# Performance work log

Measured on AMD Instinct MI355X. Metric: run time of the kernel, lower is better.

## Reference

```python
import jax, jax.numpy as jnp
import numpy as np

N, C, H, W = 2, 128, 64, 64
N_HEAD = 4
GROUPS = 16
EPS = 1e-5


def group_norm(x, scale, offset):
    # haiku GroupNorm, channels_first: normalize over (channels-in-group, h, w)
    n, c, h, w = x.shape
    xg = x.reshape(n, GROUPS, c // GROUPS, h, w)
    mu = xg.mean(axis=(2, 3, 4), keepdims=True)
    var = xg.var(axis=(2, 3, 4), keepdims=True)
    xg = (xg - mu) * jax.lax.rsqrt(var + EPS)
    return xg.reshape(n, c, h, w) * scale[None, :, None, None] + offset[None, :, None, None]


def setup_inputs() -> dict:
    key = jax.random.key(0)
    ks = jax.random.split(key, 4)
    inv_sqrt_c = 1.0 / np.sqrt(C).astype(np.float32)
    return {
        "x": jax.random.normal(ks[0], (N, C, H, W), dtype=jnp.float32),
        "w_qkv": jax.random.normal(ks[1], (C, 3 * C), dtype=jnp.float32) * inv_sqrt_c,
        "b_qkv": jnp.zeros((3 * C,), dtype=jnp.float32),
        "w_out": jax.random.normal(ks[2], (C, C), dtype=jnp.float32) * inv_sqrt_c,
        "b_out": jnp.zeros((C,), dtype=jnp.float32),
        "gn1_scale": jnp.ones((C,), dtype=jnp.float32),
        "gn1_offset": jnp.zeros((C,), dtype=jnp.float32),
        "gn2_scale": jnp.ones((C,), dtype=jnp.float32),
        "gn2_offset": jnp.zeros((C,), dtype=jnp.float32),
    }


def reference(x, w_qkv, b_qkv, w_out, b_out, gn1_scale, gn1_offset, gn2_scale, gn2_offset):
    n, c, h, w = x.shape
    dh = c // N_HEAD
    # GroupNorm (x is reassigned, so the residual uses the normalized x)
    xn = group_norm(x, gn1_scale, gn1_offset)
    # 1x1 conv qkv projection: [n, 3c, h, w]
    qkv = jnp.einsum('nchw,cd->ndhw', xn, w_qkv) + b_qkv[None, :, None, None]
    # [n, 3H, dh, hw] -> [n, 3H, hw, dh]
    qkv = jnp.swapaxes(qkv.reshape(n, N_HEAD * 3, dh, h * w), 2, 3)
    q, k, v = jnp.split(qkv, 3, axis=1)  # each [n, H, hw, dh]
    scale = dh ** (-0.25)
    # [n, H, hw, hw] attention matrix (the memory-bound core)
    att = jax.nn.softmax((q * scale) @ (jnp.swapaxes(k, 2, 3) * scale), axis=3)
    y = jnp.swapaxes(att @ v, 2, 3).reshape(n, c, h, w)
    # 1x1 conv out projection + GroupNorm + residual
    out = jnp.einsum('nchw,cd->ndhw', y, w_out) + b_out[None, :, None, None]
    return xn + group_norm(out, gn2_scale, gn2_offset)
```

## Files before the change

### kernel.cpp

```cpp
#include <hip/hip_runtime.h>
#include <hip/hip_bf16.h>
#include <math.h>

constexpr int cHW   = 4096;
constexpr int cC    = 128;
constexpr int cNH   = 4;
constexpr int cDH   = 32;
constexpr float cEPS = 1e-5f;
constexpr float cQS = 0.2550347805f;
constexpr int SPLIT = 8;

typedef short bh8 __attribute__((ext_vector_type(8)));
typedef float f4  __attribute__((ext_vector_type(4)));

static __device__ __forceinline__ unsigned short f2bf(float f) {
  union { __hip_bfloat16 h; unsigned short u; } cv;
  cv.h = __float2bfloat16(f);
  return cv.u;
}
static __device__ __forceinline__ unsigned pack2bf(float a, float b) {
  return (unsigned)f2bf(a) | ((unsigned)f2bf(b) << 16);
}
static __device__ __forceinline__ unsigned pack_trunc(float a, float b) {
  unsigned ua = __builtin_bit_cast(unsigned, a);
  unsigned ub = __builtin_bit_cast(unsigned, b);
  return (ua >> 16) | (ub & 0xffff0000u);
}
static __device__ __forceinline__ float bflo(unsigned pk) {
  return __builtin_bit_cast(float, pk << 16);
}
static __device__ __forceinline__ float bfhi(unsigned pk) {
  return __builtin_bit_cast(float, pk & 0xffff0000u);
}

__device__ __forceinline__ void block_reduce2(float& a, float& b, float* sbuf) {
  #pragma unroll
  for (int off = 32; off > 0; off >>= 1) {
    a += __shfl_down(a, off, 64);
    b += __shfl_down(b, off, 64);
  }
  int wave = threadIdx.x >> 6;
  int lane = threadIdx.x & 63;
  if (lane == 0) { sbuf[wave] = a; sbuf[4 + wave] = b; }
  __syncthreads();
  if (threadIdx.x == 0) {
    sbuf[8] = sbuf[0] + sbuf[1] + sbuf[2] + sbuf[3];
    sbuf[9] = sbuf[4] + sbuf[5] + sbuf[6] + sbuf[7];
  }
  __syncthreads();
  a = sbuf[8];
  b = sbuf[9];
}

__global__ __launch_bounds__(256)
void prep(const float* __restrict__ x, float* __restrict__ part,
          const float* __restrict__ wq, const float* __restrict__ wo,
          unsigned short* __restrict__ wqT, unsigned short* __restrict__ woT) {
  __shared__ float lds[32 * 133];
  int L = threadIdx.x;
  if (blockIdx.x < 256) {
    int ng = blockIdx.x >> 3, sl = blockIdx.x & 7;
    const float4* s4 = (const float4*)x;
    float s = 0.f, s2 = 0.f;
    #pragma unroll
    for (int i = 0; i < 4; i++) {
      int idx = i * 256 + L;
      int c = idx >> 7, tt = idx & 127;
      float4 v = s4[(size_t)(ng * 8 + c) * 1024 + sl * 128 + tt];
      s  += v.x + v.y + v.z + v.w;
      s2 += v.x*v.x + v.y*v.y + v.z*v.z + v.w*v.w;
    }
    block_reduce2(s, s2, lds);
    if (L == 0) { part[blockIdx.x * 2] = s; part[blockIdx.x * 2 + 1] = s2; }
  } else {
    int bx = blockIdx.x - 256;
    const float* src; unsigned short* dst; int W, d0;
    if (bx < 12) { src = wq; dst = wqT; W = 384; d0 = bx * 32; }
    else         { src = wo; dst = woT; W = 128; d0 = (bx - 12) * 32; }
    #pragma unroll
    for (int i = 0; i < 16; i++) {
      int c = i * 8 + (L >> 5), d = L & 31;
      lds[d * 133 + c] = src[(size_t)c * W + d0 + d];
    }
    __syncthreads();
    int d = L >> 3, ch = L & 7, c0 = ch * 16;
    unsigned pk[8];
    #pragma unroll
    for (int j = 0; j < 8; j++)
      pk[j] = pack2bf(lds[d * 133 + c0 + 2 * j], lds[d * 133 + c0 + 2 * j + 1]);
    uint4* d4 = (uint4*)(dst + (size_t)(d0 + d) * 128 + c0);
    d4[0] = make_uint4(pk[0], pk[1], pk[2], pk[3]);
    d4[1] = make_uint4(pk[4], pk[5], pk[6], pk[7]);
  }
}

__global__ __launch_bounds__(256)
void gn_stats(const float* __restrict__ src, float* __restrict__ part) {
  __shared__ float sbuf[10];
  int ng = blockIdx.x >> 3, sl = blockIdx.x & 7;
  const float4* s4 = (const float4*)src;
  float s = 0.f, s2 = 0.f;
  #pragma unroll
  for (int i = 0; i < 4; i++) {
    int idx = i * 256 + threadIdx.x;
    int c = idx >> 7, tt = idx & 127;
    float4 v = s4[(size_t)(ng * 8 + c) * 1024 + sl * 128 + tt];
    s  += v.x + v.y + v.z + v.w;
    s2 += v.x*v.x + v.y*v.y + v.z*v.z + v.w*v.w;
  }
  block_reduce2(s, s2, sbuf);
  if (threadIdx.x == 0) { part[blockIdx.x * 2] = s; part[blockIdx.x * 2 + 1] = s2; }
}

__global__ __launch_bounds__(256)
void gn1_pack(const float* __restrict__ x, const float* __restrict__ part,
              const float* __restrict__ sc, const float* __restrict__ of,
              unsigned short* __restrict__ xnB) {
  int cc = blockIdx.x, ts = blockIdx.y, n = blockIdx.z;
  int ng = n * 16 + cc;
  float s = 0.f, s2 = 0.f;
  #pragma unroll
  for (int p = 0; p < 8; p++) { s += part[(ng*8+p)*2]; s2 += part[(ng*8+p)*2+1]; }
  float mu = s * (1.0f / 32768.0f);
  float rinv = rsqrtf(s2 * (1.0f / 32768.0f) - mu * mu + cEPS);
  int t = ts * 256 + threadIdx.x;
  float v[8];
  #pragma unroll
  for (int j = 0; j < 8; j++) {
    int c = cc * 8 + j;
    float a = rinv * sc[c];
    float bo = of[c] - mu * a;
    v[j] = x[((size_t)n * cC + c) * cHW + t] * a + bo;
  }
  unsigned pk[4];
  #pragma unroll
  for (int j = 0; j < 4; j++) pk[j] = pack2bf(v[2*j], v[2*j+1]);
  ((uint4*)xnB)[(size_t)(n * 16 + cc) * cHW + t] = make_uint4(pk[0], pk[1], pk[2], pk[3]);
}

__global__ __launch_bounds__(256)
void qkv_mfma(const unsigned short* __restrict__ xnB, const unsigned short* __restrict__ wqT,
              const float* __restrict__ bq, unsigned* __restrict__ qB,
              unsigned* __restrict__ kB, unsigned* __restrict__ vI) {
  __shared__ float vbuf[64 * 36];
  const int L = threadIdx.x & 63, w = threadIdx.x >> 6;
  const int c16 = L & 15, q = L >> 4;
  const int t0 = blockIdx.x * 64, dg = blockIdx.y, n = blockIdx.z;
  const int nh = n * 4 + (dg & 3), d0 = dg * 32;
  const f4 zf = {0.f, 0.f, 0.f, 0.f};
  f4 acc0 = zf, acc1 = zf;
  const int trow = t0 + w * 16 + c16;
  #pragma unroll
  for (int ks = 0; ks < 4; ks++) {
    bh8 a  = *(const bh8*)(xnB + ((size_t)(n * 16 + ks * 4 + q) * cHW + trow) * 8);
    bh8 b0 = *(const bh8*)(wqT + (size_t)(d0 + c16) * 128 + ks * 32 + q * 8);
    bh8 b1 = *(const bh8*)(wqT + (size_t)(d0 + 16 + c16) * 128 + ks * 32 + q * 8);
    acc0 = __builtin_amdgcn_mfma_f32_16x16x32_bf16(a, b0, acc0, 0, 0, 0);
    acc1 = __builtin_amdgcn_mfma_f32_16x16x32_bf16(a, b1, acc1, 0, 0, 0);
  }
  float blo = bq[d0 + c16], bhi = bq[d0 + 16 + c16];
  if (dg < 8) {
    float scl = (dg < 4) ? cQS : 1.0f;
    unsigned* dst = (dg < 4) ? qB : kB;
    #pragma unroll
    for (int r = 0; r < 4; r++) {
      unsigned pk = pack2bf((acc0[r] + blo) * scl, (acc1[r] + bhi) * scl);
      dst[((size_t)nh * cHW + t0 + w * 16 + q * 4 + r) * 16 + c16] = pk;
    }
  } else {
    #pragma unroll
    for (int r = 0; r < 4; r++) {
      vbuf[(w * 16 + q * 4 + r) * 36 + c16]      = acc0[r] + blo;
      vbuf[(w * 16 + q * 4 + r) * 36 + 16 + c16] = acc1[r] + bhi;
    }
    __syncthreads();
    int t16 = threadIdx.x & 15, dh8 = (threadIdx.x >> 4) & 15;
    #pragma unroll
    for (int blk = 0; blk < 2; blk++)
      #pragma unroll
      for (int hh = 0; hh < 2; hh++) {
        int dh = dh8 + hh * 16;
        float lo = vbuf[(blk * 32 + t16) * 36 + dh];
        float hi = vbuf[(blk * 32 + 16 + t16) * 36 + dh];
        vI[((size_t)nh * 32 + dh) * 2048 + (size_t)(t0 / 32 + blk) * 16 + t16] = pack2bf(lo, hi);
      }
  }
}

__global__ __launch_bounds__(256)
void flash_mfma(const unsigned short* __restrict__ qB,
                const unsigned short* __restrict__ kB,
                const unsigned short* __restrict__ vI,
                unsigned* __restrict__ opart, float* __restrict__ lpart) {
  __shared__ float pbuf[4][1280];
  const int w = threadIdx.x >> 6, L = threadIdx.x & 63;
  const int c16 = L & 15, q = L >> 4;
  const int qt = blockIdx.x * 4 + w, nh = blockIdx.y, ph = blockIdx.z;
  float* pb = pbuf[w];
  const f4 zf = {0.f, 0.f, 0.f, 0.f};
  const short oneb = 0x3F80;
  const bh8 ones = {oneb, oneb, oneb, oneb, oneb, oneb, oneb, oneb};

  const unsigned short* qb = qB + ((size_t)nh * cHW + qt * 32) * cDH;
  bh8 qa[2];
  qa[0] = *(const bh8*)(qb + (size_t)c16 * cDH + q * 8);
  qa[1] = *(const bh8*)(qb + (size_t)(16 + c16) * cDH + q * 8);

  f4 o[2][2] = {{zf, zf}, {zf, zf}};
  f4 lacc[2] = {zf, zf};

  const unsigned short* kb = kB + (size_t)nh * cHW * cDH;
  const unsigned short* vb = vI + (size_t)nh * cDH * cHW;

  const int kbeg = ph * (cHW / SPLIT);
  const int kend = kbeg + cHW / SPLIT;

  for (int kt = kbeg; kt < kend; kt += 64) {
    bh8 kf[4];
    #pragma unroll
    for (int s = 0; s < 4; s++)
      kf[s] = *(const bh8*)(kb + (size_t)(kt + s*16 + c16) * cDH + q * 8);
    bh8 vf[2][2];
    #pragma unroll
    for (int ks = 0; ks < 2; ks++)
      #pragma unroll
      for (int dt = 0; dt < 2; dt++)
        vf[ks][dt] = *(const bh8*)(vb + (size_t)(dt*16 + c16) * cHW + kt + ks*32 + q*8);

    f4 sf[2][4];
    #pragma unroll
    for (int rt = 0; rt < 2; rt++)
      #pragma unroll
      for (int s = 0; s < 4; s++)
        sf[rt][s] = __builtin_amdgcn_mfma_f32_16x16x32_bf16(qa[rt], kf[s], zf, 0, 0, 0);

    #pragma unroll
    for (int rt = 0; rt < 2; rt++) {
      #pragma unroll
      for (int s = 0; s < 4; s++)
        #pragma unroll
        for (int r = 0; r < 4; r++)
          sf[rt][s][r] = __builtin_amdgcn_exp2f(sf[rt][s][r]);
      #pragma unroll
      for (int st = 0; st < 2; st++)
        #pragma unroll
        for (int r = 0; r < 4; r++) {
          unsigned pk = pack_trunc(sf[rt][2*st][r], sf[rt][2*st+1][r]);
          pb[(rt*2 + st)*320 + (q*4 + r)*20 + c16] = __builtin_bit_cast(float, pk);
        }
    }
    #pragma unroll
    for (int rt = 0; rt < 2; rt++)
      #pragma unroll
      for (int st = 0; st < 2; st++) {
        f4 praw = *(const f4*)(pb + (rt*2 + st)*320 + c16*20 + q*4);
        bh8 pa = __builtin_bit_cast(bh8, praw);
        o[rt][0] = __builtin_amdgcn_mfma_f32_16x16x32_bf16(pa, vf[st][0], o[rt][0], 0, 0, 0);
        o[rt][1] = __builtin_amdgcn_mfma_f32_16x16x32_bf16(pa, vf[st][1], o[rt][1], 0, 0, 0);
        lacc[rt] = __builtin_amdgcn_mfma_f32_16x16x32_bf16(pa, ones, lacc[rt], 0, 0, 0);
      }
  }

  size_t base_r = (size_t)ph * 32768 + (size_t)nh * cHW + (size_t)qt * 32;
  #pragma unroll
  for (int rt = 0; rt < 2; rt++)
    #pragma unroll
    for (int r = 0; r < 4; r++) {
      size_t rr = base_r + rt*16 + q*4 + r;
      if (c16 == 0) lpart[rr] = lacc[rt][r];
      opart[rr * 16 + c16] = pack_trunc(o[rt][0][r], o[rt][1][r]);
    }
}

__global__ __launch_bounds__(256)
void combine(const unsigned* __restrict__ opart, const float* __restrict__ lpart,
             unsigned* __restrict__ yB) {
  size_t r = (size_t)blockIdx.x * 256 + threadIdx.x;
  float l = 0.f;
  #pragma unroll
  for (int p = 0; p < SPLIT; p++) l += lpart[(size_t)p * 32768 + r];
  float e[32];
  #pragma unroll
  for (int j = 0; j < 32; j++) e[j] = 0.f;
  #pragma unroll
  for (int p = 0; p < SPLIT; p++) {
    const uint4* op = (const uint4*)(opart + ((size_t)p * 32768 + r) * 16);
    #pragma unroll
    for (int j = 0; j < 4; j++) {
      uint4 v = op[j];
      e[j*4+0] += bflo(v.x); e[16+j*4+0] += bfhi(v.x);
      e[j*4+1] += bflo(v.y); e[16+j*4+1] += bfhi(v.y);
      e[j*4+2] += bflo(v.z); e[16+j*4+2] += bfhi(v.z);
      e[j*4+3] += bflo(v.w); e[16+j*4+3] += bfhi(v.w);
    }
  }
  float inv = 1.0f / l;
  unsigned pk[16];
  #pragma unroll
  for (int m = 0; m < 16; m++) pk[m] = pack2bf(e[2*m] * inv, e[2*m+1] * inv);
  uint4* dst = (uint4*)(yB + r * 16);
  #pragma unroll
  for (int j = 0; j < 4; j++)
    dst[j] = make_uint4(pk[4*j], pk[4*j+1], pk[4*j+2], pk[4*j+3]);
}

__global__ __launch_bounds__(256)
void out_mfma(const unsigned short* __restrict__ yB, const unsigned short* __restrict__ woT,
              const float* __restrict__ bo, float* __restrict__ proj) {
  __shared__ float obuf[64 * 36];
  const int L = threadIdx.x & 63, w = threadIdx.x >> 6;
  const int c16 = L & 15, q = L >> 4;
  const int t0 = blockIdx.x * 64, d0 = blockIdx.y * 32, n = blockIdx.z;
  const f4 zf = {0.f, 0.f, 0.f, 0.f};
  f4 acc0 = zf, acc1 = zf;
  const int trow = t0 + w * 16 + c16;
  #pragma unroll
  for (int h = 0; h < 4; h++) {
    bh8 a  = *(const bh8*)(yB + ((size_t)(n * 4 + h) * cHW + trow) * 32 + q * 8);
    bh8 b0 = *(const bh8*)(woT + (size_t)(d0 + c16) * 128 + h * 32 + q * 8);
    bh8 b1 = *(const bh8*)(woT + (size_t)(d0 + 16 + c16) * 128 + h * 32 + q * 8);
    acc0 = __builtin_amdgcn_mfma_f32_16x16x32_bf16(a, b0, acc0, 0, 0, 0);
    acc1 = __builtin_amdgcn_mfma_f32_16x16x32_bf16(a, b1, acc1, 0, 0, 0);
  }
  float blo = bo[d0 + c16], bhi = bo[d0 + 16 + c16];
  #pragma unroll
  for (int r = 0; r < 4; r++) {
    obuf[(w * 16 + q * 4 + r) * 36 + c16]      = acc0[r] + blo;
    obuf[(w * 16 + q * 4 + r) * 36 + 16 + c16] = acc1[r] + bhi;
  }
  __syncthreads();
  int t16 = threadIdx.x & 15, d8 = (threadIdx.x >> 4) & 15;
  #pragma unroll
  for (int tc = 0; tc < 4; tc++)
    #pragma unroll
    for (int hh = 0; hh < 2; hh++) {
      int d = d8 + hh * 16;
      proj[((size_t)n * cC + d0 + d) * cHW + t0 + tc * 16 + t16] =
          obuf[(tc * 16 + t16) * 36 + d];
    }
}

__global__ __launch_bounds__(256)
void gn2_apply(const float* __restrict__ x, const float* __restrict__ proj,
               const float* __restrict__ p1, const float* __restrict__ p2,
               const float* __restrict__ s1, const float* __restrict__ o1,
               const float* __restrict__ s2, const float* __restrict__ o2,
               float* __restrict__ out) {
  int tid = blockIdx.x * 256 + threadIdx.x;
  int Cg = tid >> 8;
  int n = Cg >> 7, ch = Cg & 127, g = ch >> 3, ng = n * 16 + g;
  float sa = 0.f, sb = 0.f, ta = 0.f, tb = 0.f;
  #pragma unroll
  for (int p = 0; p < 8; p++) {
    sa += p1[(ng*8+p)*2]; sb += p1[(ng*8+p)*2+1];
    ta += p2[(ng*8+p)*2]; tb += p2[(ng*8+p)*2+1];
  }
  float mu1 = sa * (1.0f/32768.0f);
  float ri1 = rsqrtf(sb * (1.0f/32768.0f) - mu1*mu1 + cEPS);
  float a1 = ri1 * s1[ch], b1 = o1[ch] - mu1 * a1;
  float mu2 = ta * (1.0f/32768.0f);
  float ri2 = rsqrtf(tb * (1.0f/32768.0f) - mu2*mu2 + cEPS);
  float a2 = ri2 * s2[ch], b2 = o2[ch] - mu2 * a2;
  const float4* x4 = (const float4*)x;
  const float4* pr4 = (const float4*)proj;
  float4* o4 = (float4*)out;
  #pragma unroll
  for (int i = 0; i < 4; i++) {
    size_t f = (size_t)tid * 4 + i;
    float4 xv = x4[f], pv = pr4[f];
    float4 r;
    r.x = xv.x * a1 + b1 + pv.x * a2 + b2;
    r.y = xv.y * a1 + b1 + pv.y * a2 + b2;
    r.z = xv.z * a1 + b1 + pv.z * a2 + b2;
    r.w = xv.w * a1 + b1 + pv.w * a2 + b2;
    o4[f] = r;
  }
}

extern "C" void kernel_launch(void* const* d_in, const int* in_sizes, int n_in,
                              void* d_out, int out_size, void* d_ws, size_t ws_size,
                              hipStream_t stream) {
  const float* x     = (const float*)d_in[0];
  const float* w_qkv = (const float*)d_in[1];
  const float* b_qkv = (const float*)d_in[2];
  const float* w_out = (const float*)d_in[3];
  const float* b_out = (const float*)d_in[4];
  const float* g1s   = (const float*)d_in[5];
  const float* g1o   = (const float*)d_in[6];
  const float* g2s   = (const float*)d_in[7];
  const float* g2o   = (const float*)d_in[8];
  float* out = (float*)d_out;

  unsigned* qB = (unsigned*)d_ws;
  unsigned* kB = qB + 524288;
  unsigned* vI = kB + 524288;
  unsigned* yB = vI + 524288;
  unsigned short* woT = (unsigned short*)(yB + 524288);
  float* stats1 = (float*)(woT + 16384);
  float* stats2 = stats1 + 512;
  float* lpart  = stats2 + 512;
  unsigned* opart = (unsigned*)(lpart + (size_t)SPLIT * 32768);
  float* proj = (float*)opart;
  unsigned short* xnB = (unsigned short*)opart;
  unsigned short* wqT = xnB + 1048576;

  prep      <<<dim3(272),           256, 0, stream>>>(x, stats1, w_qkv, w_out, wqT, woT);
  gn1_pack  <<<dim3(16, 16, 2),     256, 0, stream>>>(x, stats1, g1s, g1o, xnB);
  qkv_mfma  <<<dim3(64, 12, 2),     256, 0, stream>>>(xnB, wqT, b_qkv, qB, kB, vI);
  flash_mfma<<<dim3(32, 8, SPLIT),  256, 0, stream>>>((const unsigned short*)qB,
                                                      (const unsigned short*)kB,
                                                      (const unsigned short*)vI,
                                                      opart, lpart);
  combine   <<<dim3(128),           256, 0, stream>>>(opart, lpart, yB);
  out_mfma  <<<dim3(64, 4, 2),      256, 0, stream>>>((const unsigned short*)yB, woT,
                                                      b_out, proj);
  gn_stats  <<<dim3(256),           256, 0, stream>>>(proj, stats2);
  gn2_apply <<<dim3(256),           256, 0, stream>>>(x, proj, stats1, stats2,
                                                      g1s, g1o, g2s, g2o, out);
}
```

Baseline: 154.4 us.

## Compute transposed scores so P feeds PV MFMA from registers without LDS

New measurement: 158.9 us. 1.03x slower.

```diff
diff --git a/kernel.cpp b/kernel.cpp
--- a/kernel.cpp
+++ b/kernel.cpp
@@ -12,6 +12,7 @@
 
 typedef short bh8 __attribute__((ext_vector_type(8)));
 typedef float f4  __attribute__((ext_vector_type(4)));
+typedef unsigned u4 __attribute__((ext_vector_type(4)));
 
 static __device__ __forceinline__ unsigned short f2bf(float f) {
   union { __hip_bfloat16 h; unsigned short u; } cv;
@@ -174,15 +175,17 @@
       vbuf[(w * 16 + q * 4 + r) * 36 + 16 + c16] = acc1[r] + bhi;
     }
     __syncthreads();
-    int t16 = threadIdx.x & 15, dh8 = (threadIdx.x >> 4) & 15;
+    int d = threadIdx.x & 15, dh8 = (threadIdx.x >> 4) & 15;
+    int Q = d >> 2, sd = d & 3;
+    int bk = (sd < 2) ? (4 * Q + 2 * sd) : (16 + 4 * Q + 2 * (sd - 2));
     #pragma unroll
     for (int blk = 0; blk < 2; blk++)
       #pragma unroll
       for (int hh = 0; hh < 2; hh++) {
         int dh = dh8 + hh * 16;
-        float lo = vbuf[(blk * 32 + t16) * 36 + dh];
-        float hi = vbuf[(blk * 32 + 16 + t16) * 36 + dh];
-        vI[((size_t)nh * 32 + dh) * 2048 + (size_t)(t0 / 32 + blk) * 16 + t16] = pack2bf(lo, hi);
+        float lo = vbuf[(blk * 32 + bk) * 36 + dh];
+        float hi = vbuf[(blk * 32 + bk + 1) * 36 + dh];
+        vI[((size_t)nh * 32 + dh) * 2048 + (size_t)(t0 / 32 + blk) * 16 + d] = pack2bf(lo, hi);
       }
   }
 }
@@ -192,22 +195,20 @@
                 const unsigned short* __restrict__ kB,
                 const unsigned short* __restrict__ vI,
                 unsigned* __restrict__ opart, float* __restrict__ lpart) {
-  __shared__ float pbuf[4][1280];
   const int w = threadIdx.x >> 6, L = threadIdx.x & 63;
   const int c16 = L & 15, q = L >> 4;
   const int qt = blockIdx.x * 4 + w, nh = blockIdx.y, ph = blockIdx.z;
-  float* pb = pbuf[w];
   const f4 zf = {0.f, 0.f, 0.f, 0.f};
   const short oneb = 0x3F80;
   const bh8 ones = {oneb, oneb, oneb, oneb, oneb, oneb, oneb, oneb};
 
   const unsigned short* qb = qB + ((size_t)nh * cHW + qt * 32) * cDH;
-  bh8 qa[2];
-  qa[0] = *(const bh8*)(qb + (size_t)c16 * cDH + q * 8);
-  qa[1] = *(const bh8*)(qb + (size_t)(16 + c16) * cDH + q * 8);
-
-  f4 o[2][2] = {{zf, zf}, {zf, zf}};
-  f4 lacc[2] = {zf, zf};
+  bh8 qfr[2];
+  qfr[0] = *(const bh8*)(qb + (size_t)c16 * cDH + q * 8);
+  qfr[1] = *(const bh8*)(qb + (size_t)(16 + c16) * cDH + q * 8);
+
+  f4 o[2][2]    = {{zf, zf}, {zf, zf}};
+  f4 lacc[2]    = {zf, zf};
 
   const unsigned short* kb = kB + (size_t)nh * cHW * cDH;
   const unsigned short* vb = vI + (size_t)nh * cDH * cHW;
@@ -215,61 +216,52 @@
   const int kbeg = ph * (cHW / SPLIT);
   const int kend = kbeg + cHW / SPLIT;
 
-  for (int kt = kbeg; kt < kend; kt += 64) {
-    bh8 kf[4];
-    #pragma unroll
-    for (int s = 0; s < 4; s++)
-      kf[s] = *(const bh8*)(kb + (size_t)(kt + s*16 + c16) * cDH + q * 8);
-    bh8 vf[2][2];
-    #pragma unroll
-    for (int ks = 0; ks < 2; ks++)
+  for (int kt = kbeg; kt < kend; kt += 32) {
+    bh8 kf0 = *(const bh8*)(kb + (size_t)(kt + c16) * cDH + q * 8);
+    bh8 kf1 = *(const bh8*)(kb + (size_t)(kt + 16 + c16) * cDH + q * 8);
+    bh8 vf0 = *(const bh8*)(vb + (size_t)c16 * cHW + kt + q * 8);
+    bh8 vf1 = *(const bh8*)(vb + (size_t)(16 + c16) * cHW + kt + q * 8);
+
+    f4 st[2][2];
+    st[0][0] = __builtin_amdgcn_mfma_f32_16x16x32_bf16(kf0, qfr[0], zf, 0, 0, 0);
+    st[0][1] = __builtin_amdgcn_mfma_f32_16x16x32_bf16(kf0, qfr[1], zf, 0, 0, 0);
+    st[1][0] = __builtin_amdgcn_mfma_f32_16x16x32_bf16(kf1, qfr[0], zf, 0, 0, 0);
+    st[1][1] = __builtin_amdgcn_mfma_f32_16x16x32_bf16(kf1, qfr[1], zf, 0, 0, 0);
+
+    #pragma unroll
+    for (int kt2 = 0; kt2 < 2; kt2++)
       #pragma unroll
-      for (int dt = 0; dt < 2; dt++)
-        vf[ks][dt] = *(const bh8*)(vb + (size_t)(dt*16 + c16) * cHW + kt + ks*32 + q*8);
-
-    f4 sf[2][4];
-    #pragma unroll
-    for (int rt = 0; rt < 2; rt++)
-      #pragma unroll
-      for (int s = 0; s < 4; s++)
-        sf[rt][s] = __builtin_amdgcn_mfma_f32_16x16x32_bf16(qa[rt], kf[s], zf, 0, 0, 0);
-
-    #pragma unroll
-    for (int rt = 0; rt < 2; rt++) {
-      #pragma unroll
-      for (int s = 0; s < 4; s++)
+      for (int qt2 = 0; qt2 < 2; qt2++)
         #pragma unroll
         for (int r = 0; r < 4; r++)
-          sf[rt][s][r] = __builtin_amdgcn_exp2f(sf[rt][s][r]);
-      #pragma unroll
-      for (int st = 0; st < 2; st++)
-        #pragma unroll
-        for (int r = 0; r < 4; r++) {
-          unsigned pk = pack_trunc(sf[rt][2*st][r], sf[rt][2*st+1][r]);
-          pb[(rt*2 + st)*320 + (q*4 + r)*20 + c16] = __builtin_bit_cast(float, pk);
-        }
-    }
-    #pragma unroll
-    for (int rt = 0; rt < 2; rt++)
-      #pragma unroll
-      for (int st = 0; st < 2; st++) {
-        f4 praw = *(const f4*)(pb + (rt*2 + st)*320 + c16*20 + q*4);
-        bh8 pa = __builtin_bit_cast(bh8, praw);
-        o[rt][0] = __builtin_amdgcn_mfma_f32_16x16x32_bf16(pa, vf[st][0], o[rt][0], 0, 0, 0);
-        o[rt][1] = __builtin_amdgcn_mfma_f32_16x16x32_bf16(pa, vf[st][1], o[rt][1], 0, 0, 0);
-        lacc[rt] = __builtin_amdgcn_mfma_f32_16x16x32_bf16(pa, ones, lacc[rt], 0, 0, 0);
-      }
+          st[kt2][qt2][r] = __builtin_amdgcn_exp2f(st[kt2][qt2][r]);
+
+    #pragma unroll
+    for (int qt2 = 0; qt2 < 2; qt2++) {
+      u4 pu;
+      pu.x = pack_trunc(st[0][qt2][0], st[0][qt2][1]);
+      pu.y = pack_trunc(st[0][qt2][2], st[0][qt2][3]);
+      pu.z = pack_trunc(st[1][qt2][0], st[1][qt2][1]);
+      pu.w = pack_trunc(st[1][qt2][2], st[1][qt2][3]);
+      bh8 pfr = __builtin_bit_cast(bh8, pu);
+      o[0][qt2] = __builtin_amdgcn_mfma_f32_16x16x32_bf16(vf0, pfr, o[0][qt2], 0, 0, 0);
+      o[1][qt2] = __builtin_amdgcn_mfma_f32_16x16x32_bf16(vf1, pfr, o[1][qt2], 0, 0, 0);
+      lacc[qt2] = __builtin_amdgcn_mfma_f32_16x16x32_bf16(ones, pfr, lacc[qt2], 0, 0, 0);
+    }
   }
 
   size_t base_r = (size_t)ph * 32768 + (size_t)nh * cHW + (size_t)qt * 32;
   #pragma unroll
-  for (int rt = 0; rt < 2; rt++)
-    #pragma unroll
-    for (int r = 0; r < 4; r++) {
-      size_t rr = base_r + rt*16 + q*4 + r;
-      if (c16 == 0) lpart[rr] = lacc[rt][r];
-      opart[rr * 16 + c16] = pack_trunc(o[rt][0][r], o[rt][1][r]);
-    }
+  for (int qt2 = 0; qt2 < 2; qt2++) {
+    size_t rr = base_r + qt2 * 16 + c16;
+    if (q == 0) lpart[rr] = lacc[qt2][0];
+    u4 pk;
+    pk.x = pack_trunc(o[0][qt2][0], o[1][qt2][0]);
+    pk.y = pack_trunc(o[0][qt2][1], o[1][qt2][1]);
+    pk.z = pack_trunc(o[0][qt2][2], o[1][qt2][2]);
+    pk.w = pack_trunc(o[0][qt2][3], o[1][qt2][3]);
+    *(u4*)(opart + rr * 16 + q * 4) = pk;
+  }
 }
 
 __global__ __launch_bounds__(256)
```
